# Kernel tuning notes

Hardware: AMD Instinct MI355X
Metric: run time of the kernel (lower is better)

The kernel has to match this reference:

```python
import jax, jax.numpy as jnp
import numpy as np

N, LH, PL = 512, 20, 10          # agents, history len, prediction len
H, E, NH, FF = 128, 64, 10, 2048  # rnn hidden, embedding, heads, ffn dim
D = H + 2                         # transformer d_model = 130
DH = D // NH                      # head dim = 13
DT = 0.1
NLAYERS = 3


def setup_inputs() -> dict:
    key = jax.random.key(0)
    ks = list(jax.random.split(key, 40))
    def rn(shape, s=0.02):
        return jax.random.normal(ks.pop(), shape, jnp.float32) * s
    Tracks = jax.random.normal(ks.pop(), (N, LH, 5), jnp.float32)
    Tracks = Tracks.at[:, :, 0].set(1.0)  # nonzero ids: all agents active every frame
    return dict(
        Tracks=Tracks,
        W_emb=rn((E, 4)), b_emb=jnp.zeros((E,), jnp.float32),
        W_ih=rn((4 * H, E)), W_hh=rn((4 * H, H)),
        b_ih=jnp.zeros((4 * H,), jnp.float32), b_hh=jnp.zeros((4 * H,), jnp.float32),
        enc_qkv_w=rn((NLAYERS, 3 * D, D)), enc_qkv_b=jnp.zeros((NLAYERS, 3 * D), jnp.float32),
        enc_out_w=rn((NLAYERS, D, D)), enc_out_b=jnp.zeros((NLAYERS, D), jnp.float32),
        enc_ff1_w=rn((NLAYERS, FF, D)), enc_ff1_b=jnp.zeros((NLAYERS, FF), jnp.float32),
        enc_ff2_w=rn((NLAYERS, D, FF)), enc_ff2_b=jnp.zeros((NLAYERS, D), jnp.float32),
        enc_ln1_s=jnp.ones((NLAYERS, D), jnp.float32), enc_ln1_b=jnp.zeros((NLAYERS, D), jnp.float32),
        enc_ln2_s=jnp.ones((NLAYERS, D), jnp.float32), enc_ln2_b=jnp.zeros((NLAYERS, D), jnp.float32),
        W_sp=rn((H, D)), b_sp=jnp.zeros((H,), jnp.float32),
        W_p1=rn((H, H)), b_p1=jnp.zeros((H,), jnp.float32),
        W_p2=rn((H, H)), b_p2=jnp.zeros((H,), jnp.float32),
        W_pl=rn((2, H)), b_pl=jnp.zeros((2,), jnp.float32),
    )


def _ln(x, s, b):
    m = jnp.mean(x, -1, keepdims=True)
    v = jnp.mean((x - m) ** 2, -1, keepdims=True)
    return (x - m) / jnp.sqrt(v + 1e-5) * s + b


def _mha(x, qkv_w, qkv_b, ow, ob):
    # x: [N, D] unbatched sequence of N agent tokens (torch unbatched semantics)
    qkv = x @ qkv_w.T + qkv_b
    q, k, v = jnp.split(qkv, 3, -1)
    def heads(t):
        return t.reshape(-1, NH, DH).transpose(1, 0, 2)  # [NH, N, DH]
    q, k, v = heads(q), heads(k), heads(v)
    scores = jnp.einsum('hnd,hmd->hnm', q, k) / jnp.sqrt(jnp.float32(DH))
    att = jax.nn.softmax(scores, -1)
    o = jnp.einsum('hnm,hmd->hnd', att, v).transpose(1, 0, 2).reshape(-1, D)
    return o @ ow.T + ob


def _forward(Tracks, W_emb, b_emb, W_ih, W_hh, b_ih, b_hh,
             enc_qkv_w, enc_qkv_b, enc_out_w, enc_out_b,
             enc_ff1_w, enc_ff1_b, enc_ff2_w, enc_ff2_b,
             enc_ln1_s, enc_ln1_b, enc_ln2_s, enc_ln2_b,
             W_sp, b_sp, W_p1, b_p1, W_p2, b_p2, W_pl, b_pl):
    def emb(x):
        return x @ W_emb.T + b_emb

    def lstm(x, h, c):  # torch LSTMCell, gate order i,f,g,o
        g = x @ W_ih.T + b_ih + h @ W_hh.T + b_hh
        i, f, gg, o = jnp.split(g, 4, -1)
        c2 = jax.nn.sigmoid(f) * c + jax.nn.sigmoid(i) * jnp.tanh(gg)
        return jax.nn.sigmoid(o) * jnp.tanh(c2), c2

    def sp(h, pos):  # sp_model: 3-layer post-norm transformer encoder + linear
        x = jnp.concatenate([h, pos], 1)  # [N, D]
        for j in range(NLAYERS):
            a = _mha(x, enc_qkv_w[j], enc_qkv_b[j], enc_out_w[j], enc_out_b[j])
            x = _ln(x + a, enc_ln1_s[j], enc_ln1_b[j])
            f = jax.nn.relu(x @ enc_ff1_w[j].T + enc_ff1_b[j]) @ enc_ff2_w[j].T + enc_ff2_b[j]
            x = _ln(x + f, enc_ln2_s[j], enc_ln2_b[j])
        return x @ W_sp.T + b_sp

    def rm_sp(inp, Sh, c):
        h2, c2 = lstm(emb(inp), Sh, c)
        return sp(h2, inp[:, :2]), c2

    n = Tracks.shape[0]
    inp0 = Tracks[:, 0, 1:]
    z = jnp.zeros((n, H), Tracks.dtype)
    h, c = lstm(emb(inp0), z, z)  # step-0 init (original processes step 0 twice)
    Sh = sp(h, inp0[:, :2])

    def step(carry, inp):
        Sh, c = carry
        Sh, c = rm_sp(inp, Sh, c)
        return (Sh, c), None

    (Sh, c), _ = jax.lax.scan(step, (Sh, c), jnp.moveaxis(Tracks[:, :, 1:], 1, 0))

    def pstep(carry, _):
        Sh, c, cf = carry
        x = jax.nn.relu(Sh @ W_p1.T + b_p1) + Sh
        x = jax.nn.relu(x @ W_p2.T + b_p2) + x
        a = x @ W_pl.T + b_pl                       # acceleration [N,2]
        v = a * DT + cf[:, 2:]                      # velocity update first (in-place order)
        pnew = a * (DT * DT / 2) + v * DT + cf[:, :2]
        out = jnp.concatenate([pnew, v], 1)
        Sh, c = rm_sp(out, Sh, c)
        return (Sh, c, out), out

    _, pre = jax.lax.scan(pstep, (Sh, c, Tracks[:, -1, 1:]), None, length=PL)
    return jnp.moveaxis(pre, 0, 1)  # [N, pre_len, 4]


def reference(Tracks, W_emb, b_emb, W_ih, W_hh, b_ih, b_hh,
              enc_qkv_w, enc_qkv_b, enc_out_w, enc_out_b,
              enc_ff1_w, enc_ff1_b, enc_ff2_w, enc_ff2_b,
              enc_ln1_s, enc_ln1_b, enc_ln2_s, enc_ln2_b,
              W_sp, b_sp, W_p1, b_p1, W_p2, b_p2, W_pl, b_pl):
    return _forward(Tracks, W_emb, b_emb, W_ih, W_hh, b_ih, b_hh,
                    enc_qkv_w, enc_qkv_b, enc_out_w, enc_out_b,
                    enc_ff1_w, enc_ff1_b, enc_ff2_w, enc_ff2_b,
                    enc_ln1_s, enc_ln1_b, enc_ln2_s, enc_ln2_b,
                    W_sp, b_sp, W_p1, b_p1, W_p2, b_p2, W_pl, b_pl)
```

## Files before the change

### kernel.cpp

```cpp
#include <hip/hip_runtime.h>


#define Nn 512
#define Dd 130
#define DP 132
#define Hh 128
#define Ee 64
#define FFf 2048
#define KG 192
#define TS 68

typedef float v4 __attribute__((ext_vector_type(4)));
typedef float v2 __attribute__((ext_vector_type(2)));

struct Args {
  const float *Tracks, *W_emb, *b_emb, *W_ih, *W_hh, *b_ih, *b_hh;
  const float *qkv_w, *qkv_b, *out_w, *out_b, *ff1_w, *ff1_b, *ff2_w, *ff2_b;
  const float *ln1_s, *ln1_b, *ln2_s, *ln2_b;
  const float *W_sp, *b_sp, *W_p1, *b_p1, *W_p2, *b_p2, *W_pl, *b_pl;
  float *X, *T, *Q, *Kb, *V, *O, *Sh, *C, *X1, *X2, *Y, *PART, *outp;
};

__device__ __forceinline__ float sigm(float x){ return 1.f/(1.f+__expf(-x)); }

#define LN_REDUCE(SCR) \
  { int row_=tid>>3, l8=tid&7; float s1=0.f, s2=0.f; \
    for (int k=0;k<17;k++){ int c=l8+8*k; if(c<Dd){ float v=(SCR)[row_*132+c]; s1+=v; s2+=v*v; } } \
    red1[row_*9+l8]=s1; red2_[row_*9+l8]=s2; } \
  __syncthreads(); \
  if (tid<64){ float s1=0.f,s2=0.f; \
    for (int k=0;k<8;k++){ s1+=red1[tid*9+k]; s2+=red2_[tid*9+k]; } \
    float m=s1/130.f; mu[tid]=m; inv[tid]=rsqrtf(s2/130.f-m*m+1e-5f); } \
  __syncthreads();

__global__ __launch_bounds__(512) void k_proj(Args a){
  int rg = blockIdx.x & 7, cs = blockIdx.x >> 3;
  int r0 = rg*64, c0 = cs*64;
  __shared__ alignas(16) float xs[Dd*TS];
  __shared__ alignas(16) float ws[Dd*TS];
  __shared__ float row[64*132];
  __shared__ float red1[64*9], red2_[64*9], mu[64], inv[64];
  int tid = threadIdx.x, cg = tid & 15, ig = tid >> 4;
  const float* f2b = a.ff2_b + 2*Dd;
  const float* lns = a.ln2_s + 2*Dd;
  const float* lnb = a.ln2_b + 2*Dd;
  for (int idx=tid; idx<64*Dd; idx+=512){ int c=idx/Dd, j=idx-c*Dd; ws[j*TS+c] = a.W_sp[(c0+c)*Dd+j]; }
  for (int idx=tid; idx<64*Dd; idx+=512){ int i=idx/Dd, j=idx-i*Dd;
    float sum = a.X[(r0+i)*DP+j] + f2b[j];
    for (int ksl=0;ksl<8;ksl++) sum += a.PART[(ksl*Nn + r0+i)*DP + j];
    row[i*132+j] = sum; }
  __syncthreads();
  LN_REDUCE(row)
  for (int idx=tid; idx<64*Dd; idx+=512){ int i=idx/Dd, j=idx-i*Dd;
    xs[j*TS+i] = (row[i*132+j]-mu[i])*inv[i]*lns[j] + lnb[j]; }
  __syncthreads();
  float acc[2][4] = {};
  const float* xp = xs + 2*ig;
  const float* wp = ws + 4*cg;
  #pragma unroll 4
  for (int j=0;j<Dd;j++){
    v2 xv = *(const v2*)(xp + j*TS);
    v4 wv = *(const v4*)(wp + j*TS);
    #pragma unroll
    for (int aa=0;aa<2;aa++)
      #pragma unroll
      for (int bb=0;bb<4;bb++) acc[aa][bb] += xv[aa]*wv[bb];
  }
  #pragma unroll
  for (int aa=0;aa<2;aa++){
    int r = r0 + 2*ig + aa, c = c0 + 4*cg;
    v4 o;
    #pragma unroll
    for (int bb=0;bb<4;bb++) o[bb] = acc[aa][bb] + a.b_sp[c+bb];
    *(v4*)&a.Sh[r*Hh+c] = o;
  }
}

__global__ __launch_bounds__(512) void k_mlp(Args a, const float* inp, const float* W, const float* b, float* outp){
  int rg = blockIdx.x & 7, cs = blockIdx.x >> 3;
  int r0 = rg*64, c0 = cs*64;
  __shared__ alignas(16) float xs[Hh*TS];
  __shared__ alignas(16) float ws[Hh*TS];
  int tid = threadIdx.x, cg = tid & 15, ig = tid >> 4;
  for (int idx=tid; idx<64*Hh; idx+=512){ int i=idx>>7, j=idx&127; xs[j*TS+i] = inp[(r0+i)*Hh+j]; }
  for (int idx=tid; idx<64*Hh; idx+=512){ int c=idx>>7, j=idx&127; ws[j*TS+c] = W[(c0+c)*Hh+j]; }
  __syncthreads();
  float acc[2][4] = {};
  const float* xp = xs + 2*ig;
  const float* wp = ws + 4*cg;
  #pragma unroll 4
  for (int j=0;j<Hh;j++){
    v2 xv = *(const v2*)(xp + j*TS);
    v4 wv = *(const v4*)(wp + j*TS);
    #pragma unroll
    for (int aa=0;aa<2;aa++)
      #pragma unroll
      for (int bb=0;bb<4;bb++) acc[aa][bb] += xv[aa]*wv[bb];
  }
  #pragma unroll
  for (int aa=0;aa<2;aa++){
    int r = r0 + 2*ig + aa, c = c0 + 4*cg;
    v4 ri = *(const v4*)&inp[r*Hh+c];
    v4 o;
    #pragma unroll
    for (int bb=0;bb<4;bb++) o[bb] = fmaxf(acc[aa][bb]+b[c+bb],0.f) + ri[bb];
    *(v4*)&outp[r*Hh+c] = o;
  }
}

__global__ __launch_bounds__(256) void k_pout(Args a, int p){
  int r0 = blockIdx.x*8;
  __shared__ float red[16*17];
  int tid = threadIdx.x;
  int o = tid & 15, kq = tid >> 4;
  int ii = o>>1, jj = o&1, r = r0+ii;
  float s = 0.f;
  for (int v=kq*8; v<kq*8+8; v++) s += a.X2[r*Hh+v]*a.W_pl[jj*Hh+v];
  red[o*17+kq] = s;
  __syncthreads();
  if (tid < 16){
    int oo=tid, i2=oo>>1, j=oo&1, rr=r0+i2;
    float av = a.b_pl[j];
    for (int k=0;k<16;k++) av += red[oo*17+k];
    float cf0, cf2;
    if (p==0){ cf0 = a.Tracks[(rr*20+19)*5+1+j]; cf2 = a.Tracks[(rr*20+19)*5+3+j]; }
    else     { cf0 = a.outp[rr*40+(p-1)*4+j];    cf2 = a.outp[rr*40+(p-1)*4+2+j]; }
    float vv = av*0.1f + cf2;
    float pn = av*0.005f + vv*0.1f + cf0;
    a.outp[rr*40+p*4+j]   = pn;
    a.outp[rr*40+p*4+2+j] = vv;
  }
}

__global__ __launch_bounds__(512) void k_gates(Args a, int xin_mode, int tstep, int p, int sh_zero){
  int rg = blockIdx.x & 7, us = blockIdx.x >> 3;
  int r0 = rg*64, u0 = us*16;
  __shared__ alignas(16) float xs[KG*TS];
  __shared__ alignas(16) float ws[KG*TS];
  __shared__ float xin[64*4];
  int tid = threadIdx.x, cg = tid & 15, ig = tid >> 4;
  for (int idx=tid; idx<64*4; idx+=512){ int i=idx>>2, j=idx&3; int r=r0+i;
    xin[i*4+j] = (xin_mode==0) ? a.Tracks[(r*20+tstep)*5+1+j] : a.outp[r*40+p*4+j]; }
  for (int idx=tid; idx<64*Hh; idx+=512){ int i=idx>>7, v=idx&127;
    xs[(Ee+v)*TS+i] = sh_zero ? 0.f : a.Sh[(r0+i)*Hh+v]; }
  for (int idx=tid; idx<64*KG; idx+=512){ int row=idx/KG, j=idx-row*KG;
    int u=row>>2, g=row&3; int wrow = g*Hh + u0 + u;
    ws[j*TS+row] = (j<Ee) ? a.W_ih[wrow*Ee+j] : a.W_hh[wrow*Hh+(j-Ee)]; }
  __syncthreads();
  for (int idx=tid; idx<64*Ee; idx+=512){ int e=idx>>6, i=idx&63;
    float s = a.b_emb[e];
    #pragma unroll
    for (int j=0;j<4;j++) s += xin[i*4+j]*a.W_emb[e*4+j];
    xs[e*TS+i] = s; }
  __syncthreads();
  float acc[2][4] = {};
  const float* xp = xs + 2*ig;
  const float* wp = ws + 4*cg;
  #pragma unroll 4
  for (int j=0;j<KG;j++){
    v2 xv = *(const v2*)(xp + j*TS);
    v4 wv = *(const v4*)(wp + j*TS);
    #pragma unroll
    for (int aa=0;aa<2;aa++)
      #pragma unroll
      for (int bb=0;bb<4;bb++) acc[aa][bb] += xv[aa]*wv[bb];
  }
  int u = u0 + cg;
  #pragma unroll
  for (int rr=0;rr<2;rr++){
    int r = r0 + 2*ig + rr;
    float gi = acc[rr][0] + a.b_ih[u]      + a.b_hh[u];
    float gf = acc[rr][1] + a.b_ih[Hh+u]   + a.b_hh[Hh+u];
    float gg = acc[rr][2] + a.b_ih[2*Hh+u] + a.b_hh[2*Hh+u];
    float go = acc[rr][3] + a.b_ih[3*Hh+u] + a.b_hh[3*Hh+u];
    float cp = sh_zero ? 0.f : a.C[r*Hh+u];
    float c2 = sigm(gf)*cp + sigm(gi)*tanhf(gg);
    a.C[r*Hh+u] = c2;
    a.X[r*DP+u] = sigm(go)*tanhf(c2);
  }
  if (us==0 && tid<128){ int i=tid>>1, jj=tid&1;
    a.X[(r0+i)*DP + Hh + jj] = xin[i*4+jj]; }
}

__global__ __launch_bounds__(512) void k_qkv(Args a, int layer){
  int rg = blockIdx.x & 7, cs = blockIdx.x >> 3;
  int r0 = rg*64, c0 = cs*64;
  __shared__ alignas(16) float xs[Dd*TS];
  __shared__ alignas(16) float ws[Dd*TS];
  const float* qw = a.qkv_w + layer*390*Dd;
  const float* qb = a.qkv_b + layer*390;
  int tid = threadIdx.x, cg = tid & 15, ig = tid >> 4;
  for (int idx=tid; idx<64*Dd; idx+=512){ int i=idx/Dd, j=idx-i*Dd; xs[j*TS+i] = a.X[(r0+i)*DP+j]; }
  for (int idx=tid; idx<64*Dd; idx+=512){ int c=idx/Dd, j=idx-c*Dd; int gc=c0+c;
    ws[j*TS+c] = (gc<390) ? qw[gc*Dd+j] : 0.f; }
  __syncthreads();
  float acc[2][4] = {};
  const float* xp = xs + 2*ig;
  const float* wp = ws + 4*cg;
  #pragma unroll 4
  for (int j=0;j<Dd;j++){
    v2 xv = *(const v2*)(xp + j*TS);
    v4 wv = *(const v4*)(wp + j*TS);
    #pragma unroll
    for (int aa=0;aa<2;aa++)
      #pragma unroll
      for (int bb=0;bb<4;bb++) acc[aa][bb] += xv[aa]*wv[bb];
  }
  #pragma unroll
  for (int aa=0;aa<2;aa++){
    int r = r0 + 2*ig + aa;
    #pragma unroll
    for (int bb=0;bb<4;bb++){
      int c = c0 + 4*cg + bb;
      if (c < 390){
        float v = acc[aa][bb] + qb[c];
        if (c < Dd)        a.Q [r*DP + c]        = v;
        else if (c < 2*Dd) a.Kb[r*DP + (c-Dd)]   = v;
        else               a.V [r*DP + (c-2*Dd)] = v;
      }
    }
  }
}

__global__ __launch_bounds__(256) void k_attn(Args a){
  int rg = blockIdx.x & 31, head = blockIdx.x >> 5;
  int r0 = rg*16, hc = head*13;
  __shared__ alignas(16) float kv[512*14];
  __shared__ alignas(16) float sc[16*516];
  __shared__ float red[16*17];
  __shared__ float rowm[16], rowsi[16];
  int tid = threadIdx.x;
  const float scale = rsqrtf(13.f);
  for (int idx=tid; idx<512*13; idx+=256){ int m=idx/13, d=idx-13*m; kv[m*14+d]=a.Kb[m*DP+hc+d]; }
  __syncthreads();
  { int ii=tid>>4, mg=tid&15;
    float q[13];
    #pragma unroll
    for (int d=0;d<13;d++) q[d]=a.Q[(r0+ii)*DP+hc+d]*scale;
    for (int k=0;k<32;k++){ int m=mg+16*k;
      float s=0.f;
      #pragma unroll
      for (int d=0;d<13;d++) s += q[d]*kv[m*14+d];
      sc[ii*516+m]=s; } }
  __syncthreads();
  for (int idx=tid; idx<512*13; idx+=256){ int m=idx/13, d=idx-13*m; kv[d*524+m]=a.V[m*DP+hc+d]; }
  { int row=tid>>4, l=tid&15; float mx=-1e30f;
    for (int k=0;k<32;k++) mx=fmaxf(mx, sc[row*516+l+16*k]);
    red[row*17+l]=mx; }
  __syncthreads();
  if (tid<16){ float mx=-1e30f; for(int k=0;k<16;k++) mx=fmaxf(mx,red[tid*17+k]); rowm[tid]=mx; }
  __syncthreads();
  { int row=tid>>4, l=tid&15; float s=0.f; float mx=rowm[row];
    for (int k=0;k<32;k++){ int m=l+16*k; float e=__expf(sc[row*516+m]-mx); sc[row*516+m]=e; s+=e; }
    red[row*17+l]=s; }
  __syncthreads();
  if (tid<16){ float s=0.f; for(int k=0;k<16;k++) s+=red[tid*17+k]; rowsi[tid]=1.f/s; }
  __syncthreads();
  if (tid<208){ int ii=tid/13, d=tid-13*ii;
    float accv=0.f;
    const float* sp = sc + ii*516;
    const float* vp = kv + d*524;
    #pragma unroll 4
    for (int mb=0;mb<128;mb++){
      v4 sv = *(const v4*)(sp + 4*mb);
      v4 vv = *(const v4*)(vp + 4*mb);
      accv += sv[0]*vv[0]+sv[1]*vv[1]+sv[2]*vv[2]+sv[3]*vv[3];
    }
    a.O[(r0+ii)*DP+hc+d]=accv*rowsi[ii]; }
}

__global__ __launch_bounds__(512) void k_oproj(Args a, int layer){
  int rg = blockIdx.x & 7, cs = blockIdx.x >> 3;
  int r0 = rg*64, c0 = cs*64;
  __shared__ alignas(16) float xs[Dd*TS];
  __shared__ alignas(16) float ws[Dd*TS];
  const float* ow = a.out_w + layer*Dd*Dd;
  const float* ob = a.out_b + layer*Dd;
  int tid = threadIdx.x, cg = tid & 15, ig = tid >> 4;
  for (int idx=tid; idx<64*Dd; idx+=512){ int i=idx/Dd, j=idx-i*Dd; xs[j*TS+i]=a.O[(r0+i)*DP+j]; }
  for (int idx=tid; idx<64*Dd; idx+=512){ int c=idx/Dd, j=idx-c*Dd; int gc=c0+c;
    ws[j*TS+c] = (gc<Dd) ? ow[gc*Dd+j] : 0.f; }
  __syncthreads();
  float acc[2][4] = {};
  const float* xp = xs + 2*ig;
  const float* wp = ws + 4*cg;
  #pragma unroll 4
  for (int j=0;j<Dd;j++){
    v2 xv = *(const v2*)(xp + j*TS);
    v4 wv = *(const v4*)(wp + j*TS);
    #pragma unroll
    for (int aa=0;aa<2;aa++)
      #pragma unroll
      for (int bb=0;bb<4;bb++) acc[aa][bb] += xv[aa]*wv[bb];
  }
  #pragma unroll
  for (int aa=0;aa<2;aa++){
    int r = r0 + 2*ig + aa;
    #pragma unroll
    for (int bb=0;bb<4;bb++){
      int c = c0 + 4*cg + bb;
      if (c < Dd) a.T[r*DP+c] = acc[aa][bb] + ob[c] + a.X[r*DP+c];
    }
  }
}

__global__ __launch_bounds__(256) void k_ln(Args a, const float* s, const float* b, int layer){
  int r0 = blockIdx.x*8;
  __shared__ float row[8*132];
  __shared__ float red1[8*33], red2[8*33];
  __shared__ float mu[8], inv[8];
  int tid = threadIdx.x, i = tid>>5, l = tid&31;
  const float* f2b = a.ff2_b + layer*Dd;
  for (int idx=tid; idx<8*Dd; idx+=256){ int ii=idx/Dd, c=idx-ii*Dd;
    float sum = a.X[(r0+ii)*DP+c] + f2b[c];
    for (int ksl=0;ksl<8;ksl++) sum += a.PART[(ksl*Nn + r0+ii)*DP + c];
    row[ii*132+c]=sum; }
  __syncthreads();
  { float s1=0.f, s2=0.f;
    for (int k=0;k<5;k++){ int c=l+32*k; if(c<Dd){ float v=row[i*132+c]; s1+=v; s2+=v*v; } }
    red1[i*33+l]=s1; red2[i*33+l]=s2; }
  __syncthreads();
  if (tid<8){ float s1=0.f,s2=0.f; for(int k=0;k<32;k++){ s1+=red1[tid*33+k]; s2+=red2[tid*33+k]; }
    float m=s1/130.f; mu[tid]=m; inv[tid]=rsqrtf(s2/130.f - m*m + 1e-5f); }
  __syncthreads();
  for (int idx=tid; idx<8*Dd; idx+=256){ int ii=idx/Dd, c=idx-ii*Dd;
    a.X[(r0+ii)*DP+c] = (row[ii*132+c]-mu[ii])*inv[ii]*s[c] + b[c]; }
}

__global__ __launch_bounds__(512) void k_ff1(Args a, int layer){
  int rg = blockIdx.x & 7, cs = blockIdx.x >> 3;
  int r0 = rg*64, c0 = cs*64;
  __shared__ alignas(16) float xs[Dd*TS];
  __shared__ alignas(16) float ws[Dd*TS];
  __shared__ float row[64*132];
  __shared__ float red1[64*9], red2_[64*9], mu[64], inv[64];
  const float* w1 = a.ff1_w + layer*FFf*Dd;
  const float* b1 = a.ff1_b + layer*FFf;
  const float* lns = a.ln1_s + layer*Dd;
  const float* lnb = a.ln1_b + layer*Dd;
  int tid = threadIdx.x, cg = tid & 15, ig = tid >> 4;
  for (int idx=tid; idx<64*Dd; idx+=512){ int c=idx/Dd, j=idx-c*Dd; ws[j*TS+c]=w1[(c0+c)*Dd+j]; }
  for (int idx=tid; idx<64*Dd; idx+=512){ int i=idx/Dd, j=idx-i*Dd; row[i*132+j]=a.T[(r0+i)*DP+j]; }
  __syncthreads();
  LN_REDUCE(row)
  for (int idx=tid; idx<64*Dd; idx+=512){ int i=idx/Dd, j=idx-i*Dd;
    float v = (row[i*132+j]-mu[i])*inv[i]*lns[j] + lnb[j];
    xs[j*TS+i] = v;
    if (cs==0) a.X[(r0+i)*DP+j] = v; }
  __syncthreads();
  float acc[2][4] = {};
  const float* xp = xs + 2*ig;
  const float* wp = ws + 4*cg;
  #pragma unroll 4
  for (int j=0;j<Dd;j++){
    v2 xv = *(const v2*)(xp + j*TS);
    v4 wv = *(const v4*)(wp + j*TS);
    #pragma unroll
    for (int aa=0;aa<2;aa++)
      #pragma unroll
      for (int bb=0;bb<4;bb++) acc[aa][bb] += xv[aa]*wv[bb];
  }
  #pragma unroll
  for (int aa=0;aa<2;aa++){
    int r = r0 + 2*ig + aa, c = c0 + 4*cg;
    v4 o;
    #pragma unroll
    for (int bb=0;bb<4;bb++) o[bb] = fmaxf(acc[aa][bb]+b1[c+bb],0.f);
    *(v4*)&a.Y[r*FFf+c] = o;
  }
}

__global__ __launch_bounds__(512) void k_ff2(Args a, int layer){
  int b = blockIdx.x;
  int rg = b & 7; int t = b >> 3; int ks = t/3; int cs = t - ks*3;
  int r0 = rg*64, c0 = cs*64, k0 = ks*256;
  __shared__ alignas(16) float xs[128*TS];
  __shared__ alignas(16) float ws[128*TS];
  const float* w2 = a.ff2_w + layer*Dd*FFf;
  int tid = threadIdx.x, cg = tid & 15, ig = tid >> 4;
  float acc[2][4] = {};
  for (int ch=0; ch<2; ch++){
    __syncthreads();
    int kb = k0 + ch*128;
    for (int idx=tid; idx<64*128; idx+=512){ int i=idx>>7, j=idx&127; xs[j*TS+i]=a.Y[(r0+i)*FFf+kb+j]; }
    for (int idx=tid; idx<64*128; idx+=512){ int c=idx>>7, j=idx&127; int gc=c0+c;
      ws[j*TS+c] = (gc<Dd) ? w2[gc*FFf+kb+j] : 0.f; }
    __syncthreads();
    const float* xp = xs + 2*ig;
    const float* wp = ws + 4*cg;
    #pragma unroll 4
    for (int j=0;j<128;j++){
      v2 xv = *(const v2*)(xp + j*TS);
      v4 wv = *(const v4*)(wp + j*TS);
      #pragma unroll
      for (int aa=0;aa<2;aa++)
        #pragma unroll
        for (int bb=0;bb<4;bb++) acc[aa][bb] += xv[aa]*wv[bb];
    }
  }
  #pragma unroll
  for (int aa=0;aa<2;aa++){
    int r = r0 + 2*ig + aa;
    #pragma unroll
    for (int bb=0;bb<4;bb++){
      int c = c0 + 4*cg + bb;
      if (c < Dd) a.PART[(ks*Nn + r)*DP + c] = acc[aa][bb];
    }
  }
}

extern "C" void kernel_launch(void* const* d_in, const int* in_sizes, int n_in,
                              void* d_out, int out_size, void* d_ws, size_t ws_size,
                              hipStream_t stream) {
  (void)in_sizes; (void)n_in; (void)out_size; (void)ws_size;
  Args A;
  const float* const* in = (const float* const*)d_in;
  A.Tracks=in[0]; A.W_emb=in[1]; A.b_emb=in[2]; A.W_ih=in[3]; A.W_hh=in[4]; A.b_ih=in[5]; A.b_hh=in[6];
  A.qkv_w=in[7]; A.qkv_b=in[8]; A.out_w=in[9]; A.out_b=in[10];
  A.ff1_w=in[11]; A.ff1_b=in[12]; A.ff2_w=in[13]; A.ff2_b=in[14];
  A.ln1_s=in[15]; A.ln1_b=in[16]; A.ln2_s=in[17]; A.ln2_b=in[18];
  A.W_sp=in[19]; A.b_sp=in[20]; A.W_p1=in[21]; A.b_p1=in[22]; A.W_p2=in[23]; A.b_p2=in[24];
  A.W_pl=in[25]; A.b_pl=in[26];
  float* ws = (float*)d_ws;
  A.X   = ws;
  A.T   = ws + 67584;
  A.Q   = ws + 135168;
  A.Kb  = ws + 202752;
  A.V   = ws + 270336;
  A.O   = ws + 337920;
  A.Sh  = ws + 405504;
  A.C   = ws + 471040;
  A.X1  = ws + 536576;
  A.X2  = ws + 602112;
  A.Y   = ws + 667648;
  A.PART= ws + 1716224;
  A.outp = (float*)d_out;

  dim3 B5(512), B2(256);
  auto enc = [&](){
    for (int l=0;l<3;l++){
      k_qkv  <<<dim3(56),  B5, 0, stream>>>(A, l);
      k_attn <<<dim3(320), B2, 0, stream>>>(A);
      k_oproj<<<dim3(24),  B5, 0, stream>>>(A, l);
      k_ff1  <<<dim3(256), B5, 0, stream>>>(A, l);
      k_ff2  <<<dim3(192), B5, 0, stream>>>(A, l);
      if (l < 2)
        k_ln <<<dim3(64),  B2, 0, stream>>>(A, A.ln2_s+l*Dd, A.ln2_b+l*Dd, l);
    }
  };

  k_gates<<<dim3(64), B5, 0, stream>>>(A, 0, 0, 0, 1);
  enc();
  for (int t=0;t<20;t++){
    k_proj <<<dim3(16), B5, 0, stream>>>(A);
    k_gates<<<dim3(64), B5, 0, stream>>>(A, 0, t, 0, 0);
    enc();
  }
  for (int p=0;p<10;p++){
    k_proj<<<dim3(16), B5, 0, stream>>>(A);
    k_mlp <<<dim3(16), B5, 0, stream>>>(A, A.Sh, A.W_p1, A.b_p1, A.X1);
    k_mlp <<<dim3(16), B5, 0, stream>>>(A, A.X1, A.W_p2, A.b_p2, A.X2);
    k_pout<<<dim3(64), B2, 0, stream>>>(A, p);
    if (p < 9){
      k_gates<<<dim3(64), B5, 0, stream>>>(A, 1, 0, p, 0);
      enc();
    }
  }
}
```

Measured before the change: 9.365 ms.

## Keep attention scores in registers, split FF2 reduction 16-way, drop LN staging buffer

Attention now computes scores and softmax in per-thread registers and does the PV product per thread over its key subset, reducing partial outputs through shared memory. This replaces a shared-memory score matrix and a 208-thread serial PV loop. FF2 doubles its grid by splitting K into 16 slices of 128, so downstream LayerNorm consumers sum 16 partials instead of 8. FF1 computes LayerNorm stats directly from global memory, which frees shared memory at the cost of extra global reads.

Measured after the change: 8.713 ms, median of 2. -7.0%, faster.

```diff
diff --git a/kernel.cpp b/kernel.cpp
--- a/kernel.cpp
+++ b/kernel.cpp
@@ -47,7 +47,7 @@
   for (int idx=tid; idx<64*Dd; idx+=512){ int c=idx/Dd, j=idx-c*Dd; ws[j*TS+c] = a.W_sp[(c0+c)*Dd+j]; }
   for (int idx=tid; idx<64*Dd; idx+=512){ int i=idx/Dd, j=idx-i*Dd;
     float sum = a.X[(r0+i)*DP+j] + f2b[j];
-    for (int ksl=0;ksl<8;ksl++) sum += a.PART[(ksl*Nn + r0+i)*DP + j];
+    for (int ksl=0;ksl<16;ksl++) sum += a.PART[(ksl*Nn + r0+i)*DP + j];
     row[i*132+j] = sum; }
   __syncthreads();
   LN_REDUCE(row)
@@ -225,48 +225,56 @@
 __global__ __launch_bounds__(256) void k_attn(Args a){
   int rg = blockIdx.x & 31, head = blockIdx.x >> 5;
   int r0 = rg*16, hc = head*13;
-  __shared__ alignas(16) float kv[512*14];
-  __shared__ alignas(16) float sc[16*516];
+  __shared__ alignas(16) float Ks[512*14];
+  __shared__ alignas(16) float Vs[512*14];
   __shared__ float red[16*17];
   __shared__ float rowm[16], rowsi[16];
+  __shared__ float red2[256*13];
   int tid = threadIdx.x;
   const float scale = rsqrtf(13.f);
-  for (int idx=tid; idx<512*13; idx+=256){ int m=idx/13, d=idx-13*m; kv[m*14+d]=a.Kb[m*DP+hc+d]; }
-  __syncthreads();
-  { int ii=tid>>4, mg=tid&15;
-    float q[13];
-    #pragma unroll
-    for (int d=0;d<13;d++) q[d]=a.Q[(r0+ii)*DP+hc+d]*scale;
-    for (int k=0;k<32;k++){ int m=mg+16*k;
-      float s=0.f;
-      #pragma unroll
-      for (int d=0;d<13;d++) s += q[d]*kv[m*14+d];
-      sc[ii*516+m]=s; } }
-  __syncthreads();
-  for (int idx=tid; idx<512*13; idx+=256){ int m=idx/13, d=idx-13*m; kv[d*524+m]=a.V[m*DP+hc+d]; }
-  { int row=tid>>4, l=tid&15; float mx=-1e30f;
-    for (int k=0;k<32;k++) mx=fmaxf(mx, sc[row*516+l+16*k]);
-    red[row*17+l]=mx; }
+  for (int idx=tid; idx<512*13; idx+=256){ int m=idx/13, d=idx-13*m; Ks[m*14+d]=a.Kb[m*DP+hc+d]; }
+  for (int idx=tid; idx<512*13; idx+=256){ int m=idx/13, d=idx-13*m; Vs[m*14+d]=a.V[m*DP+hc+d]; }
+  __syncthreads();
+  int ii = tid>>4, mg = tid&15;
+  float q[13];
+  #pragma unroll
+  for (int d=0;d<13;d++) q[d]=a.Q[(r0+ii)*DP+hc+d]*scale;
+  float p[32];
+  #pragma unroll
+  for (int k=0;k<32;k++){ int m=mg+16*k;
+    float s=0.f;
+    #pragma unroll
+    for (int d=0;d<13;d++) s += q[d]*Ks[m*14+d];
+    p[k]=s; }
+  { float mx=-1e30f;
+    #pragma unroll
+    for (int k=0;k<32;k++) mx=fmaxf(mx,p[k]);
+    red[ii*17+mg]=mx; }
   __syncthreads();
   if (tid<16){ float mx=-1e30f; for(int k=0;k<16;k++) mx=fmaxf(mx,red[tid*17+k]); rowm[tid]=mx; }
   __syncthreads();
-  { int row=tid>>4, l=tid&15; float s=0.f; float mx=rowm[row];
-    for (int k=0;k<32;k++){ int m=l+16*k; float e=__expf(sc[row*516+m]-mx); sc[row*516+m]=e; s+=e; }
-    red[row*17+l]=s; }
+  { float mx=rowm[ii]; float s=0.f;
+    #pragma unroll
+    for (int k=0;k<32;k++){ float e=__expf(p[k]-mx); p[k]=e; s+=e; }
+    red[ii*17+mg]=s; }
   __syncthreads();
   if (tid<16){ float s=0.f; for(int k=0;k<16;k++) s+=red[tid*17+k]; rowsi[tid]=1.f/s; }
-  __syncthreads();
-  if (tid<208){ int ii=tid/13, d=tid-13*ii;
-    float accv=0.f;
-    const float* sp = sc + ii*516;
-    const float* vp = kv + d*524;
-    #pragma unroll 4
-    for (int mb=0;mb<128;mb++){
-      v4 sv = *(const v4*)(sp + 4*mb);
-      v4 vv = *(const v4*)(vp + 4*mb);
-      accv += sv[0]*vv[0]+sv[1]*vv[1]+sv[2]*vv[2]+sv[3]*vv[3];
-    }
-    a.O[(r0+ii)*DP+hc+d]=accv*rowsi[ii]; }
+  float po[13];
+  #pragma unroll
+  for (int d=0;d<13;d++) po[d]=0.f;
+  #pragma unroll
+  for (int k=0;k<32;k++){ int m=mg+16*k;
+    float pv = p[k];
+    #pragma unroll
+    for (int d=0;d<13;d++) po[d] += pv*Vs[m*14+d];
+  }
+  #pragma unroll
+  for (int d=0;d<13;d++) red2[tid*13+d]=po[d];
+  __syncthreads();
+  if (tid<208){ int i2=tid/13, d=tid-13*i2;
+    float acc=0.f;
+    for (int l=0;l<16;l++) acc += red2[(i2*16+l)*13+d];
+    a.O[(r0+i2)*DP+hc+d]=acc*rowsi[i2]; }
 }
 
 __global__ __launch_bounds__(512) void k_oproj(Args a, int layer){
@@ -313,7 +321,7 @@
   const float* f2b = a.ff2_b + layer*Dd;
   for (int idx=tid; idx<8*Dd; idx+=256){ int ii=idx/Dd, c=idx-ii*Dd;
     float sum = a.X[(r0+ii)*DP+c] + f2b[c];
-    for (int ksl=0;ksl<8;ksl++) sum += a.PART[(ksl*Nn + r0+ii)*DP + c];
+    for (int ksl=0;ksl<16;ksl++) sum += a.PART[(ksl*Nn + r0+ii)*DP + c];
     row[ii*132+c]=sum; }
   __syncthreads();
   { float s1=0.f, s2=0.f;
@@ -332,7 +340,6 @@
   int r0 = rg*64, c0 = cs*64;
   __shared__ alignas(16) float xs[Dd*TS];
   __shared__ alignas(16) float ws[Dd*TS];
-  __shared__ float row[64*132];
   __shared__ float red1[64*9], red2_[64*9], mu[64], inv[64];
   const float* w1 = a.ff1_w + layer*FFf*Dd;
   const float* b1 = a.ff1_b + layer*FFf;
@@ -340,11 +347,17 @@
   const float* lnb = a.ln1_b + layer*Dd;
   int tid = threadIdx.x, cg = tid & 15, ig = tid >> 4;
   for (int idx=tid; idx<64*Dd; idx+=512){ int c=idx/Dd, j=idx-c*Dd; ws[j*TS+c]=w1[(c0+c)*Dd+j]; }
-  for (int idx=tid; idx<64*Dd; idx+=512){ int i=idx/Dd, j=idx-i*Dd; row[i*132+j]=a.T[(r0+i)*DP+j]; }
-  __syncthreads();
-  LN_REDUCE(row)
+  { int row_=tid>>3, l8=tid&7; float s1=0.f, s2=0.f;
+    const float* tr = a.T + (r0+row_)*DP;
+    for (int k=0;k<17;k++){ int c=l8+8*k; if(c<Dd){ float v=tr[c]; s1+=v; s2+=v*v; } }
+    red1[row_*9+l8]=s1; red2_[row_*9+l8]=s2; }
+  __syncthreads();
+  if (tid<64){ float s1=0.f,s2=0.f;
+    for (int k=0;k<8;k++){ s1+=red1[tid*9+k]; s2+=red2_[tid*9+k]; }
+    float m=s1/130.f; mu[tid]=m; inv[tid]=rsqrtf(s2/130.f-m*m+1e-5f); }
+  __syncthreads();
   for (int idx=tid; idx<64*Dd; idx+=512){ int i=idx/Dd, j=idx-i*Dd;
-    float v = (row[i*132+j]-mu[i])*inv[i]*lns[j] + lnb[j];
+    float v = (a.T[(r0+i)*DP+j]-mu[i])*inv[i]*lns[j] + lnb[j];
     xs[j*TS+i] = v;
     if (cs==0) a.X[(r0+i)*DP+j] = v; }
   __syncthreads();
@@ -373,30 +386,26 @@
 __global__ __launch_bounds__(512) void k_ff2(Args a, int layer){
   int b = blockIdx.x;
   int rg = b & 7; int t = b >> 3; int ks = t/3; int cs = t - ks*3;
-  int r0 = rg*64, c0 = cs*64, k0 = ks*256;
+  int r0 = rg*64, c0 = cs*64, k0 = ks*128;
   __shared__ alignas(16) float xs[128*TS];
   __shared__ alignas(16) float ws[128*TS];
   const float* w2 = a.ff2_w + layer*Dd*FFf;
   int tid = threadIdx.x, cg = tid & 15, ig = tid >> 4;
-  float acc[2][4] = {};
-  for (int ch=0; ch<2; ch++){
-    __syncthreads();
-    int kb = k0 + ch*128;
-    for (int idx=tid; idx<64*128; idx+=512){ int i=idx>>7, j=idx&127; xs[j*TS+i]=a.Y[(r0+i)*FFf+kb+j]; }
-    for (int idx=tid; idx<64*128; idx+=512){ int c=idx>>7, j=idx&127; int gc=c0+c;
-      ws[j*TS+c] = (gc<Dd) ? w2[gc*FFf+kb+j] : 0.f; }
-    __syncthreads();
-    const float* xp = xs + 2*ig;
-    const float* wp = ws + 4*cg;
-    #pragma unroll 4
-    for (int j=0;j<128;j++){
-      v2 xv = *(const v2*)(xp + j*TS);
-      v4 wv = *(const v4*)(wp + j*TS);
-      #pragma unroll
-      for (int aa=0;aa<2;aa++)
-        #pragma unroll
-        for (int bb=0;bb<4;bb++) acc[aa][bb] += xv[aa]*wv[bb];
-    }
+  for (int idx=tid; idx<64*128; idx+=512){ int i=idx>>7, j=idx&127; xs[j*TS+i]=a.Y[(r0+i)*FFf+k0+j]; }
+  for (int idx=tid; idx<64*128; idx+=512){ int c=idx>>7, j=idx&127; int gc=c0+c;
+    ws[j*TS+c] = (gc<Dd) ? w2[gc*FFf+k0+j] : 0.f; }
+  __syncthreads();
+  float acc[2][4] = {};
+  const float* xp = xs + 2*ig;
+  const float* wp = ws + 4*cg;
+  #pragma unroll 4
+  for (int j=0;j<128;j++){
+    v2 xv = *(const v2*)(xp + j*TS);
+    v4 wv = *(const v4*)(wp + j*TS);
+    #pragma unroll
+    for (int aa=0;aa<2;aa++)
+      #pragma unroll
+      for (int bb=0;bb<4;bb++) acc[aa][bb] += xv[aa]*wv[bb];
   }
   #pragma unroll
   for (int aa=0;aa<2;aa++){
@@ -443,7 +452,7 @@
       k_attn <<<dim3(320), B2, 0, stream>>>(A);
       k_oproj<<<dim3(24),  B5, 0, stream>>>(A, l);
       k_ff1  <<<dim3(256), B5, 0, stream>>>(A, l);
-      k_ff2  <<<dim3(192), B5, 0, stream>>>(A, l);
+      k_ff2  <<<dim3(384), B5, 0, stream>>>(A, l);
       if (l < 2)
         k_ln <<<dim3(64),  B2, 0, stream>>>(A, A.ln2_s+l*Dd, A.ln2_b+l*Dd, l);
     }
```
